# Performance work log

Hardware: AMD Instinct MI355X
Metric: run time of the kernel (lower is better)

The kernel has to match this reference:

```python
import jax, jax.numpy as jnp
import numpy as np
from jax import lax

B, IN_N, OUT_N, SEQ, HID = 8, 16, 16, 256, 64
NUM_C = 64 + 3  # grid_size + spline_order
EPS_LN = 1e-5


def setup_inputs():
    key = jax.random.key(0)
    k = jax.random.split(key, 8)
    f32 = jnp.float32
    return {
        "x_in": jax.random.normal(k[0], (B, IN_N, SEQ, HID), f32),
        "proj_x_prev": jax.random.normal(k[1], (B, IN_N, SEQ, HID), f32),
        "spline_weights": jax.random.normal(k[2], (IN_N, OUT_N, NUM_C), f32) * 0.1,
        "base_scales": 0.6 + 0.1 * jax.random.normal(k[3], (IN_N, OUT_N), f32),
        "tau": jax.random.normal(k[4], (IN_N, OUT_N), f32) * 0.1 + 0.1,
        "temperature": jnp.array(1.0, f32),
        "omiga": jnp.full((IN_N, OUT_N), 0.2, f32),
        "W2": jax.random.normal(k[5], (OUT_N, HID, HID), f32) / np.sqrt(HID).astype(np.float32),
        "b_param": jnp.zeros((OUT_N, SEQ, HID), f32),
        "ln_w": jnp.ones((OUT_N, HID), f32),
        "ln_b": jnp.zeros((OUT_N, HID), f32),
        "alpha": jnp.full((OUT_N,), 0.5, f32),
        "beta": jnp.ones((OUT_N,), f32),
        "gamma": jnp.full((OUT_N,), 0.5, f32),
        "theta": jnp.ones((OUT_N,), f32),
        "conv_w": jax.random.normal(k[6], (OUT_N, HID, 1, 3, 3), f32) * 0.1,
    }


def _layernorm(x, w=None, b=None):
    mu = jnp.mean(x, -1, keepdims=True)
    var = jnp.mean((x - mu) ** 2, -1, keepdims=True)
    y = (x - mu) / jnp.sqrt(var + EPS_LN)
    if w is not None:
        y = y * w + b
    return y


def _dwconv(x, w):
    # x: [b, C, 16, 16]; w: [C, 1, 3, 3]; depthwise conv, SAME padding
    return lax.conv_general_dilated(
        x, w, (1, 1), "SAME",
        dimension_numbers=("NCHW", "OIHW", "NCHW"),
        feature_group_count=x.shape[1])


def _forward(x_in, proj_x_prev, spline_weights, base_scales, tau, temperature,
             omiga, W2, b_param, ln_w, ln_b, alpha, beta, gamma, theta, conv_w):
    b, in_n, seq, feat = x_in.shape
    num_c = spline_weights.shape[-1]
    grid = jnp.linspace(-1.0, 1.0, num_c)
    h = 2.0 / (num_c - 1)

    x_energy = jnp.mean(x_in, -1)  # [b,i,s]
    x_norm = jnp.clip(
        x_energy / (jnp.max(jnp.abs(x_energy), -1, keepdims=True) + 1e-8),
        -0.99, 0.99)

    # cubic B-spline basis (masked branches -> nested where)
    dist = jnp.abs(x_norm[..., None] - grid) / h  # [b,i,s,c]
    basis = jnp.where(dist < 1.0, 2.0 / 3.0 - dist ** 2 + dist ** 3 / 2.0,
            jnp.where(dist < 2.0, (2.0 - dist) ** 3 / 6.0, jnp.zeros_like(dist)))

    base_feat = jax.nn.silu(x_norm)[:, :, None, :] * base_scales[None, :, :, None]  # [b,i,j,s]
    spline_feat = jnp.einsum("bisc,ijc->bijs", basis, spline_weights)
    edge_resp = base_feat + spline_feat
    # [b,i,j,s,f]
    activated = (edge_resp[..., None] + jnp.abs(omiga)[None, :, :, None, None]) * x_in[:, :, None]

    t_val = jnp.abs(temperature) + 1e-4
    edge_energies = jnp.mean(jnp.abs(activated), axis=(-1, -2))  # [b,i,j]
    tau_abs = jnp.abs(tau)  # [i,j]
    mask = jax.nn.sigmoid((edge_energies - tau_abs[None]) / t_val)  # [b,i,j]

    # attention kernel W1, vectorized over output neuron j
    mid = in_n // 2
    mult = edge_energies / (tau_abs[None] + 1e-8)  # [b,i,j]
    wp = proj_x_prev[:, :, None] * (mult * mask)[..., None, None]  # [b,i,j,s,d]
    d = wp.shape[-1]
    K = jnp.transpose(wp[:, :mid], (0, 2, 3, 1, 4)).reshape(b, -1, seq, mid * d)
    Q = jnp.transpose(wp[:, mid:2 * mid], (0, 2, 3, 1, 4)).reshape(b, -1, seq, mid * d)
    K, Q = _layernorm(K), _layernorm(Q)
    raw = jnp.einsum("bjsk,bjtk->bjst", K, Q) / (jnp.sqrt(jnp.float32(mid * d)) * t_val)
    W1 = jax.nn.softmax(raw, axis=-1)  # [b,j,s,s]

    # masked mean over input neurons -> per-neuron SplineWeightLayer (vectorized)
    x = jnp.mean(activated * mask[..., None, None], axis=1)  # [b,j,s,f]
    xn = _layernorm(x, ln_w[None, :, None, :], ln_b[None, :, None, :])
    x_prime = jnp.einsum("bjsf,jfo->bjso", xn, W2) + b_param[None]  # [b,j,s,o]
    o = x_prime.shape[-1]

    # depthwise 3x3 conv on 16x16 spatial view, per-j kernels
    xsp = jnp.transpose(x_prime, (1, 0, 3, 2)).reshape(-1, b, o, 16, 16)  # [j,b,o,16,16]
    w3 = jax.vmap(_dwconv)(xsp, conv_w)  # [j,b,o,16,16]
    w3 = jnp.transpose(w3.reshape(-1, b, o, seq), (1, 0, 3, 2))  # [b,j,s,o]

    eye = jnp.eye(seq, dtype=x_prime.dtype)
    ak = (jnp.abs(beta)[None, :, None, None] * W1
          + jnp.abs(alpha)[None, :, None, None] * eye[None, None])
    glob = jnp.einsum("bjst,bjto->bjso", ak, x_prime)
    combined = glob + jnp.abs(theta)[None, :, None, None] * w3
    # residual_proj is Identity since in_hidden == out_hidden
    out = combined + gamma[None, :, None, None] * x
    return out, x_prime  # both [b, out_n, seq, out_hidden]


def reference(x_in, proj_x_prev, spline_weights, base_scales, tau, temperature,
              omiga, W2, b_param, ln_w, ln_b, alpha, beta, gamma, theta, conv_w):
    return _forward(x_in, proj_x_prev, spline_weights, base_scales, tau, temperature,
                    omiga, W2, b_param, ln_w, ln_b, alpha, beta, gamma, theta, conv_w)
```

## Files before the change

### kernel.cpp

```cpp
#include <hip/hip_runtime.h>

#define EPSLN 1e-5f

typedef short bf16x8 __attribute__((ext_vector_type(8)));
typedef float f32x4 __attribute__((ext_vector_type(4)));
typedef unsigned short u16;
typedef unsigned short u16x8 __attribute__((ext_vector_type(8)));

__device__ __forceinline__ float wsum(float v){
  #pragma unroll
  for(int o=32;o;o>>=1) v += __shfl_xor(v,o);
  return v;
}
__device__ __forceinline__ float wmax(float v){
  #pragma unroll
  for(int o=32;o;o>>=1) v = fmaxf(v,__shfl_xor(v,o));
  return v;
}
__device__ __forceinline__ u16 f2bf(float f){
  unsigned int u = __float_as_uint(f);
  u = (u + 0x7FFFu + ((u>>16)&1u)) >> 16;
  return (u16)u;
}
__device__ __forceinline__ float bf2f(u16 h){
  return __uint_as_float(((unsigned int)h)<<16);
}

__global__ void __launch_bounds__(256) kA(
                   const float* __restrict__ xin, const float* __restrict__ p,
                   const float* __restrict__ W2,
                   float* __restrict__ xe, float* __restrict__ xa,
                   float* __restrict__ Sv, float* __restrict__ SSv,
                   u16* __restrict__ xinb, u16* __restrict__ phi, u16* __restrict__ plo,
                   u16* __restrict__ w2B){
  int t = threadIdx.x;
  int rl = t>>3, q = t&7;
  int row = blockIdx.x*32 + rl;
  const float4* xr = (const float4*)(xin + row*64 + q*8);
  const float4* pr = (const float4*)(p   + row*64 + q*8);
  float s1=0.f,s2=0.f,s3=0.f,s4=0.f;
  u16x8 xb, ph, pl;
  #pragma unroll
  for(int k=0;k<2;k++){
    float4 xv = xr[k];
    float4 pv = pr[k];
    s1 += xv.x+xv.y+xv.z+xv.w;
    s2 += fabsf(xv.x)+fabsf(xv.y)+fabsf(xv.z)+fabsf(xv.w);
    s3 += pv.x+pv.y+pv.z+pv.w;
    s4 += pv.x*pv.x+pv.y*pv.y+pv.z*pv.z+pv.w*pv.w;
    int o = k*4;
    xb[o+0]=f2bf(xv.x); xb[o+1]=f2bf(xv.y); xb[o+2]=f2bf(xv.z); xb[o+3]=f2bf(xv.w);
    u16 h0=f2bf(pv.x), h1=f2bf(pv.y), h2=f2bf(pv.z), h3=f2bf(pv.w);
    ph[o+0]=h0; ph[o+1]=h1; ph[o+2]=h2; ph[o+3]=h3;
    pl[o+0]=f2bf(pv.x-bf2f(h0)); pl[o+1]=f2bf(pv.y-bf2f(h1));
    pl[o+2]=f2bf(pv.z-bf2f(h2)); pl[o+3]=f2bf(pv.w-bf2f(h3));
  }
  *(u16x8*)(xinb + row*64 + q*8) = xb;
  *(u16x8*)(phi  + row*64 + q*8) = ph;
  *(u16x8*)(plo  + row*64 + q*8) = pl;
  s1 += __shfl_xor(s1,1); s1 += __shfl_xor(s1,2); s1 += __shfl_xor(s1,4);
  s2 += __shfl_xor(s2,1); s2 += __shfl_xor(s2,2); s2 += __shfl_xor(s2,4);
  s3 += __shfl_xor(s3,1); s3 += __shfl_xor(s3,2); s3 += __shfl_xor(s3,4);
  s4 += __shfl_xor(s4,1); s4 += __shfl_xor(s4,2); s4 += __shfl_xor(s4,4);
  if(q==0){ xe[row]=s1*(1.f/64.f); xa[row]=s2*(1.f/64.f); Sv[row]=s3; SSv[row]=s4; }
  if(blockIdx.x<16){
    int j = blockIdx.x;
    for(int idx=threadIdx.x; idx<4096; idx+=256){
      int f = idx>>6, o = idx&63;
      float v = W2[j*4096 + idx];
      int ks = f>>5, kb = (f>>3)&3, i = f&7;
      int nt = o>>4, col = o&15;
      int ln = kb*16 + col;
      w2B[((j*2+ks)*4 + nt)*512 + ln*8 + i] = f2bf(v);
    }
  }
}

__global__ void __launch_bounds__(256) kBE(
                   const float* __restrict__ xe, const float* __restrict__ sw,
                   const float* __restrict__ bs, const float* __restrict__ om,
                   const float* __restrict__ xa, const float* __restrict__ tau,
                   const float* __restrict__ temp,
                   float* __restrict__ er2, float* __restrict__ mask,
                   float* __restrict__ cc,
                   const u16* __restrict__ phi, const u16* __restrict__ plo,
                   float* __restrict__ G){
  __shared__ __align__(16) unsigned char shm[32768];
  int tid = threadIdx.x;
  if(blockIdx.x < 128){
    float* swL = (float*)shm;
    float* bsL = swL + 1072;
    float* omL = bsL + 16;
    float* red = omL + 16;
    float* redE= red + 4;
    int bi = blockIdx.x;
    int i = bi & 15;
    int w = tid>>6, lane = tid&63;
    for(int k=tid;k<16*67;k+=256) swL[k] = sw[i*16*67 + k];
    if(tid<16){ bsL[tid]=bs[i*16+tid]; omL[tid]=fabsf(om[i*16+tid]); }
    float v = xe[bi*256+tid];
    float m = wmax(fabsf(v));
    if(lane==0) red[w]=m;
    __syncthreads();
    m = fmaxf(fmaxf(red[0],red[1]),fmaxf(red[2],red[3]));
    float xn = v/(m+1e-8f);
    xn = fminf(fmaxf(xn,-0.99f),0.99f);
    float sil = xn/(1.f+expf(-xn));
    float vv = (xn+1.f)*33.f;
    int c0 = (int)floorf(vv)-1;
    float acc[16];
    #pragma unroll
    for(int j=0;j<16;j++) acc[j]=0.f;
    #pragma unroll
    for(int k=0;k<4;k++){
      int c = c0+k;
      if(c<0||c>66) continue;
      float d = fabsf(vv-(float)c);
      float bas = d<1.f ? (2.f/3.f - d*d + d*d*d*0.5f)
                : (d<2.f ? (2.f-d)*(2.f-d)*(2.f-d)*(1.f/6.f) : 0.f);
      #pragma unroll
      for(int j=0;j<16;j++) acc[j] += bas*swL[j*67+c];
    }
    float xav = xa[bi*256+tid];
    #pragma unroll
    for(int j=0;j<16;j++){
      float ev = sil*bsL[j] + acc[j] + omL[j];
      er2[(bi*16+j)*256+tid] = ev;
      float pe = wsum(fabsf(ev)*xav);
      if(lane==0) redE[j*4+w]=pe;
    }
    __syncthreads();
    if(tid<16){
      float e = (redE[tid*4+0]+redE[tid*4+1]+redE[tid*4+2]+redE[tid*4+3])*(1.f/256.f);
      float tv = fabsf(temp[0])+1e-4f;
      float ta = fabsf(tau[i*16+tid]);
      float mk = 1.f/(1.f+expf(-(e-ta)/tv));
      mask[bi*16+tid]=mk;
      cc[bi*16+tid]= e/(ta+1e-8f)*mk;
    }
  } else {
    u16* AfB = (u16*)shm;
    u16* BfB = AfB + 8192;
    int e = blockIdx.x - 128;
    int b = e&7, m = (e>>3)&7, sx = (e>>6)&3, ty = e>>8;
    int bm = b*8+m;
    int s0 = sx*64, t0 = ty*64;
    int row = tid>>2, dseg = tid&3;
    size_t offA = ((size_t)(b*16+m  )*256 + s0 + row)*64 + dseg*16;
    size_t offB = ((size_t)(b*16+m+8)*256 + t0 + row)*64 + dseg*16;
    int d0 = dseg*16;
    int ks0 = d0>>5, kb0 = (d0>>3)&3;
    int ks1 = (d0+8)>>5, kb1 = ((d0+8)>>3)&3;
    int lr = row&15, stile = row>>4;
    #define AOFF(h,stl,ks,ln) (((((h)*4+(stl))*2+(ks))*64 + (ln))*8)
    {
      uint4 v0 = *(const uint4*)(phi + offA);
      uint4 v1 = *(const uint4*)(phi + offA + 8);
      *(uint4*)(AfB + AOFF(0,stile,ks0,kb0*16+lr)) = v0;
      *(uint4*)(AfB + AOFF(0,stile,ks1,kb1*16+lr)) = v1;
      uint4 w0 = *(const uint4*)(plo + offA);
      uint4 w1 = *(const uint4*)(plo + offA + 8);
      *(uint4*)(AfB + AOFF(1,stile,ks0,kb0*16+lr)) = w0;
      *(uint4*)(AfB + AOFF(1,stile,ks1,kb1*16+lr)) = w1;
      uint4 x0 = *(const uint4*)(phi + offB);
      uint4 x1 = *(const uint4*)(phi + offB + 8);
      *(uint4*)(BfB + AOFF(0,stile,ks0,kb0*16+lr)) = x0;
      *(uint4*)(BfB + AOFF(0,stile,ks1,kb1*16+lr)) = x1;
      uint4 y0 = *(const uint4*)(plo + offB);
      uint4 y1 = *(const uint4*)(plo + offB + 8);
      *(uint4*)(BfB + AOFF(1,stile,ks0,kb0*16+lr)) = y0;
      *(uint4*)(BfB + AOFF(1,stile,ks1,kb1*16+lr)) = y1;
    }
    __syncthreads();
    int w = tid>>6, lane = tid&63;
    bf16x8 ah0 = *(const bf16x8*)(AfB + AOFF(0,w,0,lane));
    bf16x8 ah1 = *(const bf16x8*)(AfB + AOFF(0,w,1,lane));
    bf16x8 al0 = *(const bf16x8*)(AfB + AOFF(1,w,0,lane));
    bf16x8 al1 = *(const bf16x8*)(AfB + AOFF(1,w,1,lane));
    f32x4 acc[4];
    #pragma unroll
    for(int tt=0;tt<4;tt++) acc[tt] = (f32x4){0.f,0.f,0.f,0.f};
    #pragma unroll
    for(int tt=0;tt<4;tt++){
      bf16x8 bh0 = *(const bf16x8*)(BfB + AOFF(0,tt,0,lane));
      bf16x8 bh1 = *(const bf16x8*)(BfB + AOFF(0,tt,1,lane));
      bf16x8 bl0 = *(const bf16x8*)(BfB + AOFF(1,tt,0,lane));
      bf16x8 bl1 = *(const bf16x8*)(BfB + AOFF(1,tt,1,lane));
      acc[tt] = __builtin_amdgcn_mfma_f32_16x16x32_bf16(ah0, bh0, acc[tt], 0,0,0);
      acc[tt] = __builtin_amdgcn_mfma_f32_16x16x32_bf16(ah1, bh1, acc[tt], 0,0,0);
      acc[tt] = __builtin_amdgcn_mfma_f32_16x16x32_bf16(ah0, bl0, acc[tt], 0,0,0);
      acc[tt] = __builtin_amdgcn_mfma_f32_16x16x32_bf16(ah1, bl1, acc[tt], 0,0,0);
      acc[tt] = __builtin_amdgcn_mfma_f32_16x16x32_bf16(al0, bh0, acc[tt], 0,0,0);
      acc[tt] = __builtin_amdgcn_mfma_f32_16x16x32_bf16(al1, bh1, acc[tt], 0,0,0);
    }
    int col = lane&15, r4 = lane>>4;
    #pragma unroll
    for(int tt=0;tt<4;tt++){
      #pragma unroll
      for(int r=0;r<4;r++){
        G[((size_t)bm*256 + s0 + w*16 + r4*4 + r)*256 + t0 + tt*16 + col] = acc[tt][r];
      }
    }
    #undef AOFF
  }
}

__global__ void __launch_bounds__(256) kD(
                   const u16* __restrict__ xinb, const float* __restrict__ er2,
                   const float* __restrict__ mask, const u16* __restrict__ w2B,
                   const float* __restrict__ lnw, const float* __restrict__ lnb,
                   const float* __restrict__ bp,
                   u16* __restrict__ xoutb, float* __restrict__ xp,
                   u16* __restrict__ xpB){
  int b = blockIdx.x, j = blockIdx.y, st = blockIdx.z;
  int tid = threadIdx.x, w = tid>>6, lane = tid&63;
  __shared__ __align__(16) u16 xnS[16*64];
  __shared__ float mcL[16];
  if(tid<16) mcL[tid]=mask[(b*16+tid)*16+j];
  __syncthreads();
  float lw = lnw[j*64+lane], lb = lnb[j*64+lane];
  int bj = b*16+j;
  unsigned char* xnB = (unsigned char*)xnS;
  #pragma unroll
  for(int ri=0;ri<4;ri++){
    int sl = w*4 + ri;
    int s = st*16 + sl;
    float acc=0.f;
    #pragma unroll
    for(int i=0;i<16;i++){
      acc += er2[((b*16+i)*16+j)*256+s]*mcL[i]*bf2f(xinb[((b*16+i)*256+s)*64+lane]);
    }
    float xval = acc*(1.f/16.f);
    xoutb[((size_t)bj*256+s)*64+lane]=f2bf(xval);
    float mu = wsum(xval)*(1.f/64.f);
    float dv = xval-mu;
    float var = wsum(dv*dv)*(1.f/64.f);
    float xnv = dv*rsqrtf(var+EPSLN)*lw + lb;
    *(u16*)(xnB + ((sl*128 + lane*2) ^ ((sl&7)<<4))) = f2bf(xnv);
  }
  __syncthreads();
  f32x4 acc = {0.f,0.f,0.f,0.f};
  int m = lane&15, kb = lane>>4;
  #pragma unroll
  for(int ks=0;ks<2;ks++){
    bf16x8 a = *(const bf16x8*)(xnB + ((m*128 + ks*64 + kb*16) ^ ((m&7)<<4)));
    bf16x8 bfr = *(const bf16x8*)(w2B + ((j*2+ks)*4 + w)*512 + lane*8);
    acc = __builtin_amdgcn_mfma_f32_16x16x32_bf16(a, bfr, acc, 0, 0, 0);
  }
  int f = w*16 + m;
  u16 pk[4];
  #pragma unroll
  for(int r=0;r<4;r++){
    int si = kb*4 + r;
    int s = st*16 + si;
    float xpr = acc[r] + bp[((size_t)j*256+s)*64+f];
    xp[((size_t)bj*256+s)*64+f] = xpr;
    pk[r] = f2bf(xpr);
  }
  int s0 = st*16 + kb*4;
  int flat = ((s0>>5)*4 + w)*512 + ((s0>>3)&3)*128 + m*8 + (s0&7);
  *(ushort4*)(xpB + (size_t)bj*16384 + flat) = *(ushort4*)pk;
}

__global__ void __launch_bounds__(256) kF(
    const float* __restrict__ G, const float* __restrict__ cc,
    const float* __restrict__ Sv, const float* __restrict__ SSv,
    const float* __restrict__ xp, const u16* __restrict__ xpB,
    const float* __restrict__ cw,
    const u16* __restrict__ xarrb, const float* __restrict__ temp,
    const float* __restrict__ alpha, const float* __restrict__ beta,
    const float* __restrict__ gamma_, const float* __restrict__ theta,
    float* __restrict__ out){
  int b = blockIdx.x, jp = blockIdx.y, st = blockIdx.z;
  int j0 = jp*2, j1 = j0+1;
  int tid = threadIdx.x, w = tid>>6, lane = tid&63;
  __shared__ __align__(16) unsigned char ovl[26112];
  __shared__ float mKL[2][256], rKL[2][256];
  __shared__ __align__(16) float mQL[2][256], rQL[2][256];
  unsigned char* prB0 = ovl;
  unsigned char* prB1 = ovl + 8192;
  float* xpT = (float*)ovl;
  float tv = fabsf(temp[0])+1e-4f;
  float inv = 1.f/(sqrtf(512.f)*tv);
  float ck0[8],cq0[8],ck1[8],cq1[8],aM0[8],aM1[8];
  #pragma unroll
  for(int m=0;m<8;m++){
    ck0[m]=cc[(b*16+m)*16+j0];  cq0[m]=cc[(b*16+m+8)*16+j0];
    ck1[m]=cc[(b*16+m)*16+j1];  cq1[m]=cc[(b*16+m+8)*16+j1];
    aM0[m]=ck0[m]*cq0[m];       aM1[m]=ck1[m]*cq1[m];
  }
  {
    int t = tid;
    float sk0=0,ssk0=0,sq0=0,ssq0=0,sk1=0,ssk1=0,sq1=0,ssq1=0;
    #pragma unroll
    for(int m=0;m<8;m++){
      float svk = Sv [(b*16+m)*256+t];
      float ssvk= SSv[(b*16+m)*256+t];
      float svq = Sv [(b*16+m+8)*256+t];
      float ssvq= SSv[(b*16+m+8)*256+t];
      sk0 += ck0[m]*svk;  ssk0 += ck0[m]*ck0[m]*ssvk;
      sq0 += cq0[m]*svq;  ssq0 += cq0[m]*cq0[m]*ssvq;
      sk1 += ck1[m]*svk;  ssk1 += ck1[m]*ck1[m]*ssvk;
      sq1 += cq1[m]*svq;  ssq1 += cq1[m]*cq1[m]*ssvq;
    }
    float mk0 = sk0*(1.f/512.f), mk1 = sk1*(1.f/512.f);
    float mq0 = sq0*(1.f/512.f), mq1 = sq1*(1.f/512.f);
    mKL[0][t]=mk0; rKL[0][t]=rsqrtf(ssk0*(1.f/512.f)-mk0*mk0+EPSLN);
    mKL[1][t]=mk1; rKL[1][t]=rsqrtf(ssk1*(1.f/512.f)-mk1*mk1+EPSLN);
    mQL[0][t]=mq0; rQL[0][t]=rsqrtf(ssq0*(1.f/512.f)-mq0*mq0+EPSLN);
    mQL[1][t]=mq1; rQL[1][t]=rsqrtf(ssq1*(1.f/512.f)-mq1*mq1+EPSLN);
  }
  __syncthreads();
  int bj0 = b*16+j0, bj1 = b*16+j1;
  const float* Gb = G + (size_t)(b*8)*65536;
  float4 mQ40 = *(const float4*)&mQL[0][lane*4];
  float4 rQ40 = *(const float4*)&rQL[0][lane*4];
  float4 mQ41 = *(const float4*)&mQL[1][lane*4];
  float4 rQ41 = *(const float4*)&rQL[1][lane*4];
  #pragma unroll
  for(int q=0;q<4;q++){
    int si = w*4+q;
    int s = st*16 + si;
    f32x4 dot0 = {0.f,0.f,0.f,0.f}, dot1 = {0.f,0.f,0.f,0.f};
    #pragma unroll
    for(int m=0;m<8;m++){
      f32x4 g4 = *(const f32x4*)(Gb + (size_t)m*65536 + s*256 + lane*4);
      dot0 += aM0[m]*g4;
      dot1 += aM1[m]*g4;
    }
    {
      float mKs = 512.f*mKL[0][s], rKs = rKL[0][s];
      float e0 = expf((dot0[0] - mKs*mQ40.x)*rKs*rQ40.x*inv);
      float e1 = expf((dot0[1] - mKs*mQ40.y)*rKs*rQ40.y*inv);
      float e2 = expf((dot0[2] - mKs*mQ40.z)*rKs*rQ40.z*inv);
      float e3 = expf((dot0[3] - mKs*mQ40.w)*rKs*rQ40.w*inv);
      float isf = 1.f/wsum(e0+e1+e2+e3);
      u16 pk[4] = {f2bf(e0*isf), f2bf(e1*isf), f2bf(e2*isf), f2bf(e3*isf)};
      *(ushort4*)(prB0 + ((si*512 + lane*8) ^ ((si&7)<<4))) = *(ushort4*)pk;
    }
    {
      float mKs = 512.f*mKL[1][s], rKs = rKL[1][s];
      float e0 = expf((dot1[0] - mKs*mQ41.x)*rKs*rQ41.x*inv);
      float e1 = expf((dot1[1] - mKs*mQ41.y)*rKs*rQ41.y*inv);
      float e2 = expf((dot1[2] - mKs*mQ41.z)*rKs*rQ41.z*inv);
      float e3 = expf((dot1[3] - mKs*mQ41.w)*rKs*rQ41.w*inv);
      float isf = 1.f/wsum(e0+e1+e2+e3);
      u16 pk[4] = {f2bf(e0*isf), f2bf(e1*isf), f2bf(e2*isf), f2bf(e3*isf)};
      *(ushort4*)(prB1 + ((si*512 + lane*8) ^ ((si&7)<<4))) = *(ushort4*)pk;
    }
  }
  __syncthreads();
  int m_ = lane&15, kb = lane>>4;
  f32x4 acc0 = {0.f,0.f,0.f,0.f}, acc1 = {0.f,0.f,0.f,0.f};
  const u16* xpB0 = xpB + (size_t)bj0*16384;
  const u16* xpB1 = xpB + (size_t)bj1*16384;
  #pragma unroll
  for(int ks=0;ks<8;ks++){
    int aoff = (m_*512 + ks*64 + kb*16) ^ ((m_&7)<<4);
    int boff = ((ks*4 + w)*64 + lane)*8;
    bf16x8 a0 = *(const bf16x8*)(prB0 + aoff);
    bf16x8 a1 = *(const bf16x8*)(prB1 + aoff);
    acc0 = __builtin_amdgcn_mfma_f32_16x16x32_bf16(a0, *(const bf16x8*)(xpB0 + boff), acc0, 0,0,0);
    acc1 = __builtin_amdgcn_mfma_f32_16x16x32_bf16(a1, *(const bf16x8*)(xpB1 + boff), acc1, 0,0,0);
  }
  __syncthreads();
  for(int idx4 = tid; idx4 < 1536; idx4 += 256){
    int jj = idx4 / 768;
    int rem = idx4 - jj*768;
    int rr_i = rem >> 8;
    int pos = rem & 255;
    int ci = pos>>4, f4 = pos&15;
    int grow = st - 1 + rr_i;
    float4 v = {0.f,0.f,0.f,0.f};
    if(grow>=0 && grow<16){
      v = *(const float4*)(xp + ((size_t)(b*16+j0+jj)*256 + grow*16 + ci)*64 + f4*4);
    }
    *(float4*)(xpT + ((jj*3+rr_i)*16+ci)*68 + f4*4) = v;
  }
  __syncthreads();
  int f = w*16 + m_;
  #pragma unroll
  for(int jj=0;jj<2;jj++){
    int j = j0+jj;
    int bj = b*16+j;
    f32x4 acc = jj ? acc1 : acc0;
    float al = fabsf(alpha[j]), be=fabsf(beta[j]), th=fabsf(theta[j]), ga=gamma_[j];
    const float* wq = cw + (j*64+f)*9;
    float w0=wq[0],w1=wq[1],w2=wq[2],w3v=wq[3],w4=wq[4],w5=wq[5],w6=wq[6],w7=wq[7],w8=wq[8];
    #pragma unroll
    for(int r=0;r<4;r++){
      int si = kb*4 + r;
      int s = st*16 + si;
      float gl = acc[r];
      float cv=0.f;
      #pragma unroll
      for(int dr=0;dr<3;dr++){
        float kw0 = dr==0?w0:(dr==1?w3v:w6);
        float kw1 = dr==0?w1:(dr==1?w4:w7);
        float kw2 = dr==0?w2:(dr==1?w5:w8);
        const float* rowp = xpT + ((jj*3+dr)*16)*68;
        if(si>0)  cv += rowp[(si-1)*68+f]*kw0;
                  cv += rowp[(si  )*68+f]*kw1;
        if(si<15) cv += rowp[(si+1)*68+f]*kw2;
      }
      float diag = xpT[((jj*3+1)*16+si)*68+f];
      size_t gi = ((size_t)bj*256+s)*64+f;
      out[gi] = be*gl + al*diag + th*cv + ga*bf2f(xarrb[gi]);
    }
  }
}

extern "C" void kernel_launch(void* const* d_in, const int* in_sizes, int n_in,
                              void* d_out, int out_size, void* d_ws, size_t ws_size,
                              hipStream_t stream) {
  const float* xin = (const float*)d_in[0];
  const float* pxp = (const float*)d_in[1];
  const float* sw  = (const float*)d_in[2];
  const float* bs  = (const float*)d_in[3];
  const float* tau = (const float*)d_in[4];
  const float* temp= (const float*)d_in[5];
  const float* om  = (const float*)d_in[6];
  const float* W2  = (const float*)d_in[7];
  const float* bp  = (const float*)d_in[8];
  const float* lnw = (const float*)d_in[9];
  const float* lnb = (const float*)d_in[10];
  const float* alpha=(const float*)d_in[11];
  const float* beta= (const float*)d_in[12];
  const float* gam = (const float*)d_in[13];
  const float* theta=(const float*)d_in[14];
  const float* cw  = (const float*)d_in[15];
  float* outp = (float*)d_out;
  float* xpo  = outp + 2097152;

  float* ws  = (float*)d_ws;
  float* xe  = ws;
  float* xa  = xe + 32768;
  float* Sv  = xa + 32768;
  float* SSv = Sv + 32768;
  float* er2 = SSv + 32768;
  float* mask= er2 + 524288;
  float* ccv = mask + 2048;
  float* Gv  = ccv + 2048;
  u16* xvb = (u16*)(Gv + 4194304);
  u16* xpB = xvb + 2097152;
  u16* w2B = xpB + 2097152;
  u16* xinb= w2B + 65536;
  u16* phi = xinb + 2097152;
  u16* plo = phi + 2097152;

  kA<<<1024,256,0,stream>>>(xin,pxp,W2,xe,xa,Sv,SSv,xinb,phi,plo,w2B);
  kBE<<<1152,256,0,stream>>>(xe,sw,bs,om,xa,tau,temp,er2,mask,ccv,phi,plo,Gv);
  kD<<<dim3(8,16,16),256,0,stream>>>(xinb,er2,mask,w2B,lnw,lnb,bp,xvb,xpo,xpB);
  kF<<<dim3(8,8,16),256,0,stream>>>(Gv,ccv,Sv,SSv,xpo,xpB,cw,xvb,temp,
                                    alpha,beta,gam,theta,outp);
}
```

Before: 62.03 us.

## Regroup four kernels into three by merging independent stages into shared launches

Moves the spline/energy blocks into the first kernel, where they recompute the row mean and abs-mean directly from x_in instead of reading intermediates written by a prior launch. The Gram-matrix MFMA blocks and the layernorm/W2 projection blocks now share one launch, removing one kernel boundary. In kF, the per-row key stats are kept only for the block's own 16 rows, and all stats live inside the overlay shared buffer to cut LDS use. The cost is that the energy blocks re-read all of x_in with an uncoalesced per-thread row walk, and the merged launches mix heterogeneous block types.

Result: slower. 67.63 us (+9.0%).

```diff
diff --git a/kernel.cpp b/kernel.cpp
--- a/kernel.cpp
+++ b/kernel.cpp
@@ -26,79 +26,77 @@
   return __uint_as_float(((unsigned int)h)<<16);
 }
 
-__global__ void __launch_bounds__(256) kA(
-                   const float* __restrict__ xin, const float* __restrict__ p,
-                   const float* __restrict__ W2,
-                   float* __restrict__ xe, float* __restrict__ xa,
-                   float* __restrict__ Sv, float* __restrict__ SSv,
-                   u16* __restrict__ xinb, u16* __restrict__ phi, u16* __restrict__ plo,
-                   u16* __restrict__ w2B){
-  int t = threadIdx.x;
-  int rl = t>>3, q = t&7;
-  int row = blockIdx.x*32 + rl;
-  const float4* xr = (const float4*)(xin + row*64 + q*8);
-  const float4* pr = (const float4*)(p   + row*64 + q*8);
-  float s1=0.f,s2=0.f,s3=0.f,s4=0.f;
-  u16x8 xb, ph, pl;
-  #pragma unroll
-  for(int k=0;k<2;k++){
-    float4 xv = xr[k];
-    float4 pv = pr[k];
-    s1 += xv.x+xv.y+xv.z+xv.w;
-    s2 += fabsf(xv.x)+fabsf(xv.y)+fabsf(xv.z)+fabsf(xv.w);
-    s3 += pv.x+pv.y+pv.z+pv.w;
-    s4 += pv.x*pv.x+pv.y*pv.y+pv.z*pv.z+pv.w*pv.w;
-    int o = k*4;
-    xb[o+0]=f2bf(xv.x); xb[o+1]=f2bf(xv.y); xb[o+2]=f2bf(xv.z); xb[o+3]=f2bf(xv.w);
-    u16 h0=f2bf(pv.x), h1=f2bf(pv.y), h2=f2bf(pv.z), h3=f2bf(pv.w);
-    ph[o+0]=h0; ph[o+1]=h1; ph[o+2]=h2; ph[o+3]=h3;
-    pl[o+0]=f2bf(pv.x-bf2f(h0)); pl[o+1]=f2bf(pv.y-bf2f(h1));
-    pl[o+2]=f2bf(pv.z-bf2f(h2)); pl[o+3]=f2bf(pv.w-bf2f(h3));
-  }
-  *(u16x8*)(xinb + row*64 + q*8) = xb;
-  *(u16x8*)(phi  + row*64 + q*8) = ph;
-  *(u16x8*)(plo  + row*64 + q*8) = pl;
-  s1 += __shfl_xor(s1,1); s1 += __shfl_xor(s1,2); s1 += __shfl_xor(s1,4);
-  s2 += __shfl_xor(s2,1); s2 += __shfl_xor(s2,2); s2 += __shfl_xor(s2,4);
-  s3 += __shfl_xor(s3,1); s3 += __shfl_xor(s3,2); s3 += __shfl_xor(s3,4);
-  s4 += __shfl_xor(s4,1); s4 += __shfl_xor(s4,2); s4 += __shfl_xor(s4,4);
-  if(q==0){ xe[row]=s1*(1.f/64.f); xa[row]=s2*(1.f/64.f); Sv[row]=s3; SSv[row]=s4; }
-  if(blockIdx.x<16){
-    int j = blockIdx.x;
-    for(int idx=threadIdx.x; idx<4096; idx+=256){
-      int f = idx>>6, o = idx&63;
-      float v = W2[j*4096 + idx];
-      int ks = f>>5, kb = (f>>3)&3, i = f&7;
-      int nt = o>>4, col = o&15;
-      int ln = kb*16 + col;
-      w2B[((j*2+ks)*4 + nt)*512 + ln*8 + i] = f2bf(v);
-    }
-  }
-}
-
-__global__ void __launch_bounds__(256) kBE(
-                   const float* __restrict__ xe, const float* __restrict__ sw,
-                   const float* __restrict__ bs, const float* __restrict__ om,
-                   const float* __restrict__ xa, const float* __restrict__ tau,
-                   const float* __restrict__ temp,
-                   float* __restrict__ er2, float* __restrict__ mask,
-                   float* __restrict__ cc,
-                   const u16* __restrict__ phi, const u16* __restrict__ plo,
-                   float* __restrict__ G){
-  __shared__ __align__(16) unsigned char shm[32768];
+__global__ void __launch_bounds__(256) k1(
+    const float* __restrict__ xin, const float* __restrict__ pxp,
+    const float* __restrict__ W2,  const float* __restrict__ sw,
+    const float* __restrict__ bs,  const float* __restrict__ om,
+    const float* __restrict__ tau, const float* __restrict__ temp,
+    float* __restrict__ Sv, float* __restrict__ SSv,
+    u16* __restrict__ xinb, u16* __restrict__ phi, u16* __restrict__ plo,
+    u16* __restrict__ w2B,
+    float* __restrict__ er2, float* __restrict__ mask, float* __restrict__ cc){
+  __shared__ float shmF[1172];
   int tid = threadIdx.x;
-  if(blockIdx.x < 128){
-    float* swL = (float*)shm;
+  if(blockIdx.x < 1024){
+    int rl = tid>>3, q = tid&7;
+    int row = blockIdx.x*32 + rl;
+    const float4* xr = (const float4*)(xin + row*64 + q*8);
+    const float4* pr = (const float4*)(pxp + row*64 + q*8);
+    float s3=0.f,s4=0.f;
+    u16x8 xb, ph, pl;
+    #pragma unroll
+    for(int k=0;k<2;k++){
+      float4 xv = xr[k];
+      float4 pv = pr[k];
+      s3 += pv.x+pv.y+pv.z+pv.w;
+      s4 += pv.x*pv.x+pv.y*pv.y+pv.z*pv.z+pv.w*pv.w;
+      int o = k*4;
+      xb[o+0]=f2bf(xv.x); xb[o+1]=f2bf(xv.y); xb[o+2]=f2bf(xv.z); xb[o+3]=f2bf(xv.w);
+      u16 h0=f2bf(pv.x), h1=f2bf(pv.y), h2=f2bf(pv.z), h3=f2bf(pv.w);
+      ph[o+0]=h0; ph[o+1]=h1; ph[o+2]=h2; ph[o+3]=h3;
+      pl[o+0]=f2bf(pv.x-bf2f(h0)); pl[o+1]=f2bf(pv.y-bf2f(h1));
+      pl[o+2]=f2bf(pv.z-bf2f(h2)); pl[o+3]=f2bf(pv.w-bf2f(h3));
+    }
+    *(u16x8*)(xinb + row*64 + q*8) = xb;
+    *(u16x8*)(phi  + row*64 + q*8) = ph;
+    *(u16x8*)(plo  + row*64 + q*8) = pl;
+    s3 += __shfl_xor(s3,1); s3 += __shfl_xor(s3,2); s3 += __shfl_xor(s3,4);
+    s4 += __shfl_xor(s4,1); s4 += __shfl_xor(s4,2); s4 += __shfl_xor(s4,4);
+    if(q==0){ Sv[row]=s3; SSv[row]=s4; }
+    if(blockIdx.x<16){
+      int j = blockIdx.x;
+      for(int idx=tid; idx<4096; idx+=256){
+        int f = idx>>6, o = idx&63;
+        float v = W2[j*4096 + idx];
+        int ks = f>>5, kb = (f>>3)&3, i = f&7;
+        int nt = o>>4, col = o&15;
+        int ln = kb*16 + col;
+        w2B[((j*2+ks)*4 + nt)*512 + ln*8 + i] = f2bf(v);
+      }
+    }
+  } else {
+    float* swL = shmF;
     float* bsL = swL + 1072;
     float* omL = bsL + 16;
     float* red = omL + 16;
     float* redE= red + 4;
-    int bi = blockIdx.x;
+    int bi = blockIdx.x - 1024;
     int i = bi & 15;
     int w = tid>>6, lane = tid&63;
     for(int k=tid;k<16*67;k+=256) swL[k] = sw[i*16*67 + k];
     if(tid<16){ bsL[tid]=bs[i*16+tid]; omL[tid]=fabsf(om[i*16+tid]); }
-    float v = xe[bi*256+tid];
+    float xs=0.f, xas=0.f;
+    {
+      const float4* xr = (const float4*)(xin + ((size_t)bi*256 + tid)*64);
+      #pragma unroll
+      for(int k=0;k<16;k++){
+        float4 v4 = xr[k];
+        xs  += v4.x+v4.y+v4.z+v4.w;
+        xas += fabsf(v4.x)+fabsf(v4.y)+fabsf(v4.z)+fabsf(v4.w);
+      }
+    }
+    float v   = xs *(1.f/64.f);
+    float xav = xas*(1.f/64.f);
     float m = wmax(fabsf(v));
     if(lane==0) red[w]=m;
     __syncthreads();
@@ -121,7 +119,6 @@
       #pragma unroll
       for(int j=0;j<16;j++) acc[j] += bas*swL[j*67+c];
     }
-    float xav = xa[bi*256+tid];
     #pragma unroll
     for(int j=0;j<16;j++){
       float ev = sil*bsL[j] + acc[j] + omL[j];
@@ -138,10 +135,22 @@
       mask[bi*16+tid]=mk;
       cc[bi*16+tid]= e/(ta+1e-8f)*mk;
     }
-  } else {
+  }
+}
+
+__global__ void __launch_bounds__(256) k2(
+    const u16* __restrict__ phi, const u16* __restrict__ plo, float* __restrict__ G,
+    const u16* __restrict__ xinb, const float* __restrict__ er2,
+    const float* __restrict__ mask, const u16* __restrict__ w2B,
+    const float* __restrict__ lnw, const float* __restrict__ lnb,
+    const float* __restrict__ bp,
+    u16* __restrict__ xvb, float* __restrict__ xp, u16* __restrict__ xpB){
+  __shared__ __align__(16) unsigned char shm[32768];
+  int tid = threadIdx.x;
+  if(blockIdx.x < 1024){
     u16* AfB = (u16*)shm;
     u16* BfB = AfB + 8192;
-    int e = blockIdx.x - 128;
+    int e = blockIdx.x;
     int b = e&7, m = (e>>3)&7, sx = (e>>6)&3, ty = e>>8;
     int bm = b*8+m;
     int s0 = sx*64, t0 = ty*64;
@@ -202,64 +211,57 @@
       }
     }
     #undef AOFF
-  }
-}
-
-__global__ void __launch_bounds__(256) kD(
-                   const u16* __restrict__ xinb, const float* __restrict__ er2,
-                   const float* __restrict__ mask, const u16* __restrict__ w2B,
-                   const float* __restrict__ lnw, const float* __restrict__ lnb,
-                   const float* __restrict__ bp,
-                   u16* __restrict__ xoutb, float* __restrict__ xp,
-                   u16* __restrict__ xpB){
-  int b = blockIdx.x, j = blockIdx.y, st = blockIdx.z;
-  int tid = threadIdx.x, w = tid>>6, lane = tid&63;
-  __shared__ __align__(16) u16 xnS[16*64];
-  __shared__ float mcL[16];
-  if(tid<16) mcL[tid]=mask[(b*16+tid)*16+j];
-  __syncthreads();
-  float lw = lnw[j*64+lane], lb = lnb[j*64+lane];
-  int bj = b*16+j;
-  unsigned char* xnB = (unsigned char*)xnS;
-  #pragma unroll
-  for(int ri=0;ri<4;ri++){
-    int sl = w*4 + ri;
-    int s = st*16 + sl;
-    float acc=0.f;
-    #pragma unroll
-    for(int i=0;i<16;i++){
-      acc += er2[((b*16+i)*16+j)*256+s]*mcL[i]*bf2f(xinb[((b*16+i)*256+s)*64+lane]);
-    }
-    float xval = acc*(1.f/16.f);
-    xoutb[((size_t)bj*256+s)*64+lane]=f2bf(xval);
-    float mu = wsum(xval)*(1.f/64.f);
-    float dv = xval-mu;
-    float var = wsum(dv*dv)*(1.f/64.f);
-    float xnv = dv*rsqrtf(var+EPSLN)*lw + lb;
-    *(u16*)(xnB + ((sl*128 + lane*2) ^ ((sl&7)<<4))) = f2bf(xnv);
-  }
-  __syncthreads();
-  f32x4 acc = {0.f,0.f,0.f,0.f};
-  int m = lane&15, kb = lane>>4;
-  #pragma unroll
-  for(int ks=0;ks<2;ks++){
-    bf16x8 a = *(const bf16x8*)(xnB + ((m*128 + ks*64 + kb*16) ^ ((m&7)<<4)));
-    bf16x8 bfr = *(const bf16x8*)(w2B + ((j*2+ks)*4 + w)*512 + lane*8);
-    acc = __builtin_amdgcn_mfma_f32_16x16x32_bf16(a, bfr, acc, 0, 0, 0);
-  }
-  int f = w*16 + m;
-  u16 pk[4];
-  #pragma unroll
-  for(int r=0;r<4;r++){
-    int si = kb*4 + r;
-    int s = st*16 + si;
-    float xpr = acc[r] + bp[((size_t)j*256+s)*64+f];
-    xp[((size_t)bj*256+s)*64+f] = xpr;
-    pk[r] = f2bf(xpr);
-  }
-  int s0 = st*16 + kb*4;
-  int flat = ((s0>>5)*4 + w)*512 + ((s0>>3)&3)*128 + m*8 + (s0&7);
-  *(ushort4*)(xpB + (size_t)bj*16384 + flat) = *(ushort4*)pk;
+  } else {
+    int idx = blockIdx.x - 1024;
+    int b = idx&7, j = (idx>>3)&15, st = idx>>7;
+    int w = tid>>6, lane = tid&63;
+    u16* xnS = (u16*)shm;
+    float* mcL = (float*)(shm + 2048);
+    if(tid<16) mcL[tid]=mask[(b*16+tid)*16+j];
+    __syncthreads();
+    float lw = lnw[j*64+lane], lb = lnb[j*64+lane];
+    int bj = b*16+j;
+    unsigned char* xnB = (unsigned char*)xnS;
+    #pragma unroll
+    for(int ri=0;ri<4;ri++){
+      int sl = w*4 + ri;
+      int s = st*16 + sl;
+      float acc=0.f;
+      #pragma unroll
+      for(int i=0;i<16;i++){
+        acc += er2[((b*16+i)*16+j)*256+s]*mcL[i]*bf2f(xinb[((b*16+i)*256+s)*64+lane]);
+      }
+      float xval = acc*(1.f/16.f);
+      xvb[((size_t)bj*256+s)*64+lane]=f2bf(xval);
+      float mu = wsum(xval)*(1.f/64.f);
+      float dv = xval-mu;
+      float var = wsum(dv*dv)*(1.f/64.f);
+      float xnv = dv*rsqrtf(var+EPSLN)*lw + lb;
+      *(u16*)(xnB + ((sl*128 + lane*2) ^ ((sl&7)<<4))) = f2bf(xnv);
+    }
+    __syncthreads();
+    f32x4 acc = {0.f,0.f,0.f,0.f};
+    int m = lane&15, kb = lane>>4;
+    #pragma unroll
+    for(int ks=0;ks<2;ks++){
+      bf16x8 a = *(const bf16x8*)(xnB + ((m*128 + ks*64 + kb*16) ^ ((m&7)<<4)));
+      bf16x8 bfr = *(const bf16x8*)(w2B + ((j*2+ks)*4 + w)*512 + lane*8);
+      acc = __builtin_amdgcn_mfma_f32_16x16x32_bf16(a, bfr, acc, 0, 0, 0);
+    }
+    int f = w*16 + m;
+    u16 pk[4];
+    #pragma unroll
+    for(int r=0;r<4;r++){
+      int si = kb*4 + r;
+      int s = st*16 + si;
+      float xpr = acc[r] + bp[((size_t)j*256+s)*64+f];
+      xp[((size_t)bj*256+s)*64+f] = xpr;
+      pk[r] = f2bf(xpr);
+    }
+    int s0 = st*16 + kb*4;
+    int flat = ((s0>>5)*4 + w)*512 + ((s0>>3)&3)*128 + m*8 + (s0&7);
+    *(ushort4*)(xpB + (size_t)bj*16384 + flat) = *(ushort4*)pk;
+  }
 }
 
 __global__ void __launch_bounds__(256) kF(
@@ -275,11 +277,15 @@
   int j0 = jp*2, j1 = j0+1;
   int tid = threadIdx.x, w = tid>>6, lane = tid&63;
   __shared__ __align__(16) unsigned char ovl[26112];
-  __shared__ float mKL[2][256], rKL[2][256];
-  __shared__ __align__(16) float mQL[2][256], rQL[2][256];
   unsigned char* prB0 = ovl;
   unsigned char* prB1 = ovl + 8192;
-  float* xpT = (float*)ovl;
+  float* mQL0 = (float*)(ovl + 16384);
+  float* rQL0 = (float*)(ovl + 17408);
+  float* mQL1 = (float*)(ovl + 18432);
+  float* rQL1 = (float*)(ovl + 19456);
+  float* mK2  = (float*)(ovl + 20480);
+  float* rK2  = (float*)(ovl + 20608);
+  float* xpT  = (float*)ovl;
   float tv = fabsf(temp[0])+1e-4f;
   float inv = 1.f/(sqrtf(512.f)*tv);
   float ck0[8],cq0[8],ck1[8],cq1[8],aM0[8],aM1[8];
@@ -303,20 +309,23 @@
       sk1 += ck1[m]*svk;  ssk1 += ck1[m]*ck1[m]*ssvk;
       sq1 += cq1[m]*svq;  ssq1 += cq1[m]*cq1[m]*ssvq;
     }
-    float mk0 = sk0*(1.f/512.f), mk1 = sk1*(1.f/512.f);
     float mq0 = sq0*(1.f/512.f), mq1 = sq1*(1.f/512.f);
-    mKL[0][t]=mk0; rKL[0][t]=rsqrtf(ssk0*(1.f/512.f)-mk0*mk0+EPSLN);
-    mKL[1][t]=mk1; rKL[1][t]=rsqrtf(ssk1*(1.f/512.f)-mk1*mk1+EPSLN);
-    mQL[0][t]=mq0; rQL[0][t]=rsqrtf(ssq0*(1.f/512.f)-mq0*mq0+EPSLN);
-    mQL[1][t]=mq1; rQL[1][t]=rsqrtf(ssq1*(1.f/512.f)-mq1*mq1+EPSLN);
+    mQL0[t]=mq0; rQL0[t]=rsqrtf(ssq0*(1.f/512.f)-mq0*mq0+EPSLN);
+    mQL1[t]=mq1; rQL1[t]=rsqrtf(ssq1*(1.f/512.f)-mq1*mq1+EPSLN);
+    if((t>>4)==st){
+      int si = t&15;
+      float mk0 = sk0*(1.f/512.f), mk1 = sk1*(1.f/512.f);
+      mK2[si]   =mk0; rK2[si]   =rsqrtf(ssk0*(1.f/512.f)-mk0*mk0+EPSLN);
+      mK2[16+si]=mk1; rK2[16+si]=rsqrtf(ssk1*(1.f/512.f)-mk1*mk1+EPSLN);
+    }
   }
   __syncthreads();
   int bj0 = b*16+j0, bj1 = b*16+j1;
   const float* Gb = G + (size_t)(b*8)*65536;
-  float4 mQ40 = *(const float4*)&mQL[0][lane*4];
-  float4 rQ40 = *(const float4*)&rQL[0][lane*4];
-  float4 mQ41 = *(const float4*)&mQL[1][lane*4];
-  float4 rQ41 = *(const float4*)&rQL[1][lane*4];
+  float4 mQ40 = *(const float4*)&mQL0[lane*4];
+  float4 rQ40 = *(const float4*)&rQL0[lane*4];
+  float4 mQ41 = *(const float4*)&mQL1[lane*4];
+  float4 rQ41 = *(const float4*)&rQL1[lane*4];
   #pragma unroll
   for(int q=0;q<4;q++){
     int si = w*4+q;
@@ -329,7 +338,7 @@
       dot1 += aM1[m]*g4;
     }
     {
-      float mKs = 512.f*mKL[0][s], rKs = rKL[0][s];
+      float mKs = 512.f*mK2[si], rKs = rK2[si];
       float e0 = expf((dot0[0] - mKs*mQ40.x)*rKs*rQ40.x*inv);
       float e1 = expf((dot0[1] - mKs*mQ40.y)*rKs*rQ40.y*inv);
       float e2 = expf((dot0[2] - mKs*mQ40.z)*rKs*rQ40.z*inv);
@@ -339,7 +348,7 @@
       *(ushort4*)(prB0 + ((si*512 + lane*8) ^ ((si&7)<<4))) = *(ushort4*)pk;
     }
     {
-      float mKs = 512.f*mKL[1][s], rKs = rKL[1][s];
+      float mKs = 512.f*mK2[16+si], rKs = rK2[16+si];
       float e0 = expf((dot1[0] - mKs*mQ41.x)*rKs*rQ41.x*inv);
       float e1 = expf((dot1[1] - mKs*mQ41.y)*rKs*rQ41.y*inv);
       float e2 = expf((dot1[2] - mKs*mQ41.z)*rKs*rQ41.z*inv);
@@ -433,9 +442,7 @@
   float* xpo  = outp + 2097152;
 
   float* ws  = (float*)d_ws;
-  float* xe  = ws;
-  float* xa  = xe + 32768;
-  float* Sv  = xa + 32768;
+  float* Sv  = ws;
   float* SSv = Sv + 32768;
   float* er2 = SSv + 32768;
   float* mask= er2 + 524288;
@@ -448,9 +455,9 @@
   u16* phi = xinb + 2097152;
   u16* plo = phi + 2097152;
 
-  kA<<<1024,256,0,stream>>>(xin,pxp,W2,xe,xa,Sv,SSv,xinb,phi,plo,w2B);
-  kBE<<<1152,256,0,stream>>>(xe,sw,bs,om,xa,tau,temp,er2,mask,ccv,phi,plo,Gv);
-  kD<<<dim3(8,16,16),256,0,stream>>>(xinb,er2,mask,w2B,lnw,lnb,bp,xvb,xpo,xpB);
+  k1<<<1152,256,0,stream>>>(xin,pxp,W2,sw,bs,om,tau,temp,
+                            Sv,SSv,xinb,phi,plo,w2B,er2,mask,ccv);
+  k2<<<3072,256,0,stream>>>(phi,plo,Gv,xinb,er2,mask,w2B,lnw,lnb,bp,xvb,xpo,xpB);
   kF<<<dim3(8,8,16),256,0,stream>>>(Gv,ccv,Sv,SSv,xpo,xpB,cw,xvb,temp,
                                     alpha,beta,gam,theta,outp);
 }
```
